# Kernel optimization log

Measured on AMD Instinct MI355X. Metric: run time of the kernel, lower is better.

## Reference

```python
import jax, jax.numpy as jnp
import numpy as np
from jax import lax

B, C, W, H = 32, 64, 32, 32
HEADS, RED = 4, 16
D = C // HEADS


def setup_inputs() -> dict:
    key = jax.random.key(0)
    ks = jax.random.split(key, 16)
    s = 0.05
    return {
        "x": jax.random.normal(ks[0], (B, C, W, H), jnp.float32),
        "Wq": jax.random.normal(ks[1], (C, C), jnp.float32) * s,
        "bq": jnp.zeros((C,), jnp.float32),
        "Wk": jax.random.normal(ks[2], (C, C), jnp.float32) * s,
        "bk": jnp.zeros((C,), jnp.float32),
        "Wv": jax.random.normal(ks[3], (C, C), jnp.float32) * s,
        "bv": jnp.zeros((C,), jnp.float32),
        "rel_h": jax.random.normal(ks[4], (1, HEADS, D, 1, H), jnp.float32),
        "rel_w": jax.random.normal(ks[5], (1, HEADS, D, W, 1), jnp.float32),
        "ln_g": jnp.ones((C, W, H), jnp.float32),
        "ln_b": jnp.zeros((C, W, H), jnp.float32),
        "ca_w1": jax.random.normal(ks[6], (C // RED, C), jnp.float32) * s,
        "ca_b1": jnp.zeros((C // RED,), jnp.float32),
        "ca_w2": jax.random.normal(ks[7], (C, C // RED), jnp.float32) * s,
        "ca_b2": jnp.zeros((C,), jnp.float32),
        "sa_w": jax.random.normal(ks[8], (1, 2, 7, 7), jnp.float32) * s,
        "sa_b": jnp.zeros((1,), jnp.float32),
    }


def reference(x, Wq, bq, Wk, bk, Wv, bv, rel_h, rel_w, ln_g, ln_b,
              ca_w1, ca_b1, ca_w2, ca_b2, sa_w, sa_b):
    b, c, w, h = x.shape
    n = w * h
    d = c // HEADS

    def conv1x1(t, wt, bt):
        return jnp.einsum('bchw,oc->bohw', t, wt) + bt[None, :, None, None]

    # ---- MHSA branch ----
    q = conv1x1(x, Wq, bq).reshape(b, HEADS, d, n)
    k = conv1x1(x, Wk, bk).reshape(b, HEADS, d, n)
    v = conv1x1(x, Wv, bv).reshape(b, HEADS, d, n)
    cc = jnp.einsum('bhdi,bhdj->bhij', q, k)                  # content-content
    pos = (rel_h + rel_w).reshape(1, HEADS, d, n)              # [1,H,d,N]
    cp = jnp.einsum('zhdi,bhdj->bhij', pos, q)                 # content-position
    att = jax.nn.softmax(cc + cp, axis=-1)                     # [b,H,N,N]
    out = jnp.einsum('bhdj,bhij->bhdi', v, att).reshape(b, c, w, h)
    # LayerNorm over (C,W,H)
    mu = jnp.mean(out, axis=(1, 2, 3), keepdims=True)
    var = jnp.var(out, axis=(1, 2, 3), keepdims=True)
    ln = (out - mu) * lax.rsqrt(var + 1e-5) * ln_g[None] + ln_b[None]
    mhsa = ln + x

    # ---- CBAM branch ----
    avg = jnp.mean(x, axis=(2, 3))                             # [b,c]
    mx = jnp.max(x, axis=(2, 3))

    def mlp(f):
        hid = jax.nn.relu(jnp.einsum('bc,oc->bo', f, ca_w1) + ca_b1)
        return jnp.einsum('bc,oc->bo', hid, ca_w2) + ca_b2

    ch_att = jax.nn.sigmoid(mlp(avg) + mlp(mx))[:, :, None, None]
    xc = ch_att * x
    feat = jnp.stack([jnp.mean(xc, axis=1), jnp.max(xc, axis=1)], axis=1)  # [b,2,w,h]
    sp = lax.conv_general_dilated(feat, sa_w, (1, 1), 'SAME',
                                  dimension_numbers=('NCHW', 'OIHW', 'NCHW'))
    sp = sp + sa_b[None, :, None, None]
    cbam = jax.nn.sigmoid(sp) * xc

    return mhsa + cbam + x
```

## Files before the change

### kernel.cpp

```cpp
#include <hip/hip_runtime.h>

#define BB 32
#define CC 64
#define WW 32
#define HHT 32
#define NH 4
#define DHD 16
#define NN 1024
#define LOG2E 1.4426950408889634f

typedef __attribute__((ext_vector_type(8))) short bf16x8;
typedef __attribute__((ext_vector_type(4))) float f32x4;

__device__ __forceinline__ float wave_sum(float v) {
#pragma unroll
  for (int off = 32; off > 0; off >>= 1) v += __shfl_down(v, off, 64);
  return v;
}
__device__ __forceinline__ float wave_max(float v) {
#pragma unroll
  for (int off = 32; off > 0; off >>= 1) v = fmaxf(v, __shfl_down(v, off, 64));
  return v;
}
__device__ __forceinline__ unsigned bf16pair(float lo, float hi) {
  unsigned a = __float_as_uint(lo), b = __float_as_uint(hi);
  a += 0x7FFFu + ((a >> 16) & 1u);
  b += 0x7FFFu + ((b >> 16) & 1u);
  return (a >> 16) | (b & 0xFFFF0000u);
}
__device__ __forceinline__ short bf16s(float f) {
  unsigned a = __float_as_uint(f);
  a += 0x7FFFu + ((a >> 16) & 1u);
  return (short)(a >> 16);
}

__global__ __launch_bounds__(256) void qkv_kernel(
    const float* __restrict__ x,
    const float* __restrict__ Wq, const float* __restrict__ bq,
    const float* __restrict__ Wk, const float* __restrict__ bk,
    const float* __restrict__ Wv, const float* __restrict__ bv,
    short* __restrict__ KQ, short* __restrict__ Vb, float* __restrict__ lnzero)
{
  __shared__ __align__(16) short Ws[192 * 72];
  const int tid = threadIdx.x;
  const int b = blockIdx.y, nt = blockIdx.x;

  if (tid < 192) {
    const int m = tid >> 4, dd = tid & 15;
    const int mat = m >> 2, h = m & 3;
    const float* src = (mat == 0 ? Wk : (mat == 1 ? Wq : Wv)) + (h * 16 + dd) * CC;
    const float scale = (mat == 0) ? LOG2E : 1.f;
    short* dst = Ws + tid * 72;
#pragma unroll
    for (int c8 = 0; c8 < 8; ++c8) {
      const float4 f0 = *reinterpret_cast<const float4*>(src + c8 * 8);
      const float4 f1 = *reinterpret_cast<const float4*>(src + c8 * 8 + 4);
      uint4 u;
      u.x = bf16pair(f0.x*scale, f0.y*scale); u.y = bf16pair(f0.z*scale, f0.w*scale);
      u.z = bf16pair(f1.x*scale, f1.y*scale); u.w = bf16pair(f1.z*scale, f1.w*scale);
      *reinterpret_cast<uint4*>(dst + c8 * 8) = u;
    }
  }
  if (blockIdx.x == 0 && blockIdx.y == 0 && tid < 64) lnzero[tid] = 0.f;
  __syncthreads();

  const int wid = tid >> 6, lane = tid & 63, Q = lane >> 4, il = lane & 15;
  const int n = nt * 64 + wid * 16 + il;
  const float* xb = x + (size_t)b * CC * NN;

  union { bf16x8 s; unsigned u[4]; } bfr[2];
#pragma unroll
  for (int half = 0; half < 2; ++half) {
#pragma unroll
    for (int p = 0; p < 4; ++p) {
      const int c0 = 32 * half + 8 * Q + 2 * p;
      const float f0 = xb[(size_t)c0 * NN + n];
      const float f1 = xb[(size_t)(c0 + 1) * NN + n];
      bfr[half].u[p] = bf16pair(f0, f1);
    }
  }

  const f32x4 zero4 = {0.f, 0.f, 0.f, 0.f};
  f32x4 acc[12];
#pragma unroll
  for (int m = 0; m < 12; ++m) {
    const short* wr = Ws + (m * 16 + il) * 72;
    const bf16x8 a0 = *reinterpret_cast<const bf16x8*>(wr + 8 * Q);
    const bf16x8 a1 = *reinterpret_cast<const bf16x8*>(wr + 32 + 8 * Q);
    acc[m] = __builtin_amdgcn_mfma_f32_16x16x32_bf16(a0, bfr[0].s, zero4, 0, 0, 0);
    acc[m] = __builtin_amdgcn_mfma_f32_16x16x32_bf16(a1, bfr[1].s, acc[m], 0, 0, 0);
  }

#pragma unroll
  for (int m = 0; m < 12; ++m) {
    const int mat = m >> 2, h = m & 3;
    const float bsc = (mat == 0) ? LOG2E : 1.f;
    const float4 bias = *reinterpret_cast<const float4*>(
        (mat == 0 ? bk : (mat == 1 ? bq : bv)) + h * 16 + 4 * Q);
    const float v0 = acc[m][0] + bias.x*bsc, v1 = acc[m][1] + bias.y*bsc;
    const float v2 = acc[m][2] + bias.z*bsc, v3 = acc[m][3] + bias.w*bsc;
    if (mat < 2) {
      uint2 pk;
      pk.x = bf16pair(v0, v1); pk.y = bf16pair(v2, v3);
      *reinterpret_cast<uint2*>(KQ + ((size_t)(b * NH + h) * NN + n) * 32 +
                                (mat == 0 ? 0 : 16) + 4 * Q) = pk;
    } else {
      short* vb = Vb + ((size_t)(b * NH + h) * 16 + 4 * Q) * NN + n;
      vb[0]            = bf16s(v0);
      vb[(size_t)NN]   = bf16s(v1);
      vb[2*(size_t)NN] = bf16s(v2);
      vb[3*(size_t)NN] = bf16s(v3);
    }
  }
}

__global__ __launch_bounds__(256, 4) void flash_kernel(
    const short* __restrict__ KQ, const short* __restrict__ Vb,
    const float* __restrict__ rel_h, const float* __restrict__ rel_w,
    float* __restrict__ attnout, float* __restrict__ lnsum, float* __restrict__ lnsum2)
{
  const int tid = threadIdx.x;
  const int wid = tid >> 6, lane = tid & 63;
  const int Q = lane >> 4, il = lane & 15;
  const int bh = blockIdx.x;
  const int h = bh & 3, b = bh >> 2;
  const int ibase = blockIdx.y * 128 + wid * 32;

  bf16x8 bfrag[2];
#pragma unroll
  for (int g2 = 0; g2 < 2; ++g2) {
    const int i = ibase + g2*16 + il;
    if (Q < 2) {
      bfrag[g2] = *reinterpret_cast<const bf16x8*>(KQ + ((size_t)bh*NN + i)*32 + 16 + 8*Q);
    } else {
      const int wrow = i >> 5, hcol = i & 31;
      union { bf16x8 s; unsigned u[4]; } t;
#pragma unroll
      for (int p = 0; p < 4; ++p) {
        const int d0 = 8*(Q-2) + 2*p;
        const float f0 = LOG2E*(rel_h[(h*DHD + d0)*HHT + hcol] + rel_w[(h*DHD + d0)*WW + wrow]);
        const float f1 = LOG2E*(rel_h[(h*DHD + d0+1)*HHT + hcol] + rel_w[(h*DHD + d0+1)*WW + wrow]);
        t.u[p] = bf16pair(f0, f1);
      }
      bfrag[g2] = t.s;
    }
  }

  const short* KQb = KQ + (size_t)bh*NN*32;
  const short* Vbb = Vb + ((size_t)bh*16 + il)*NN;
  const f32x4 zero4 = {0.f, 0.f, 0.f, 0.f};
  f32x4 acc[2]  = {zero4, zero4};
  f32x4 lacc[2] = {zero4, zero4};
  union { bf16x8 s; unsigned u[4]; } ones;
  ones.u[0] = ones.u[1] = ones.u[2] = ones.u[3] = 0x3F803F80u;

  bf16x8 agc[4]; uint2 vloc[2], vhic[2];
#pragma unroll
  for (int g = 0; g < 4; ++g)
    agc[g] = *reinterpret_cast<const bf16x8*>(KQb + (size_t)(16*g + il)*32 + 8*Q);
#pragma unroll
  for (int hh = 0; hh < 2; ++hh) {
    const short* vp = Vbb + 32*hh + 4*Q;
    vloc[hh] = *reinterpret_cast<const uint2*>(vp);
    vhic[hh] = *reinterpret_cast<const uint2*>(vp + 16);
  }

  for (int jt = 0; jt < NN; jt += 64) {
    const int jn = (jt + 64) & (NN - 1);
    bf16x8 agn[4]; uint2 vlon[2], vhin[2];
#pragma unroll
    for (int g = 0; g < 4; ++g)
      agn[g] = *reinterpret_cast<const bf16x8*>(KQb + (size_t)(jn + 16*g + il)*32 + 8*Q);
#pragma unroll
    for (int hh = 0; hh < 2; ++hh) {
      const short* vp = Vbb + jn + 32*hh + 4*Q;
      vlon[hh] = *reinterpret_cast<const uint2*>(vp);
      vhin[hh] = *reinterpret_cast<const uint2*>(vp + 16);
    }

    union { bf16x8 s; unsigned u[4]; } bv0, bv1;
    bv0.u[0] = vloc[0].x; bv0.u[1] = vloc[0].y; bv0.u[2] = vhic[0].x; bv0.u[3] = vhic[0].y;
    bv1.u[0] = vloc[1].x; bv1.u[1] = vloc[1].y; bv1.u[2] = vhic[1].x; bv1.u[3] = vhic[1].y;

#pragma unroll
    for (int g2 = 0; g2 < 2; ++g2) {
      unsigned pk[4][2];
#pragma unroll
      for (int g = 0; g < 4; ++g) {
        const f32x4 s = __builtin_amdgcn_mfma_f32_16x16x32_bf16(agc[g], bfrag[g2], zero4, 0, 0, 0);
        const float p0 = __builtin_amdgcn_exp2f(s[0]);
        const float p1 = __builtin_amdgcn_exp2f(s[1]);
        const float p2 = __builtin_amdgcn_exp2f(s[2]);
        const float p3 = __builtin_amdgcn_exp2f(s[3]);
        pk[g][0] = bf16pair(p0, p1);
        pk[g][1] = bf16pair(p2, p3);
      }
#pragma unroll
      for (int hh = 0; hh < 2; ++hh) {
        union { bf16x8 s; unsigned u[4]; } ap;
        ap.u[0] = pk[2*hh][0];   ap.u[1] = pk[2*hh][1];
        ap.u[2] = pk[2*hh+1][0]; ap.u[3] = pk[2*hh+1][1];
        acc[g2]  = __builtin_amdgcn_mfma_f32_16x16x32_bf16(ap.s, hh ? bv1.s : bv0.s, acc[g2], 0, 0, 0);
        lacc[g2] = __builtin_amdgcn_mfma_f32_16x16x32_bf16(ap.s, ones.s, lacc[g2], 0, 0, 0);
      }
    }
#pragma unroll
    for (int g = 0; g < 4; ++g) agc[g] = agn[g];
#pragma unroll
    for (int hh = 0; hh < 2; ++hh) { vloc[hh] = vlon[hh]; vhic[hh] = vhin[hh]; }
  }

  float s1 = 0.f, s2 = 0.f;
#pragma unroll
  for (int g2 = 0; g2 < 2; ++g2) {
#pragma unroll
    for (int r = 0; r < 4; ++r) {
      const float v = acc[g2][r] / lacc[g2][r];
      const int ig = ibase + g2*16 + 4*Q + r;
      attnout[((size_t)b*CC + h*DHD + il)*NN + ig] = v;
      s1 += v; s2 += v*v;
    }
  }
  s1 = wave_sum(s1); s2 = wave_sum(s2);
  __shared__ float r1[4], r2[4];
  if (lane == 0) { r1[wid] = s1; r2[wid] = s2; }
  __syncthreads();
  if (tid == 0) {
    atomicAdd(&lnsum[b],  r1[0]+r1[1]+r1[2]+r1[3]);
    atomicAdd(&lnsum2[b], r2[0]+r2[1]+r2[2]+r2[3]);
  }
}

__global__ __launch_bounds__(256) void cbamstats_kernel(
    const float* __restrict__ x, float* __restrict__ avg, float* __restrict__ mx)
{
  const int bc = blockIdx.x, tid = threadIdx.x;
  const float* p = x + (size_t)bc*NN;
  float s = 0.f, m = -3.0e38f;
  for (int u = tid; u < NN; u += 256) { const float v = p[u]; s += v; m = fmaxf(m, v); }
  s = wave_sum(s); m = wave_max(m);
  __shared__ float rs[4], rm[4];
  const int wid = tid >> 6, lane = tid & 63;
  if (lane == 0) { rs[wid] = s; rm[wid] = m; }
  __syncthreads();
  if (tid == 0) {
    avg[bc] = (rs[0]+rs[1]+rs[2]+rs[3]) * (1.f/NN);
    mx[bc]  = fmaxf(fmaxf(rm[0], rm[1]), fmaxf(rm[2], rm[3]));
  }
}

__global__ __launch_bounds__(256) void mlpfeat_kernel(
    const float* __restrict__ x, const float* __restrict__ avg, const float* __restrict__ mxv,
    const float* __restrict__ w1, const float* __restrict__ b1,
    const float* __restrict__ w2, const float* __restrict__ b2,
    float* __restrict__ chv, float* __restrict__ feat)
{
  const int b = blockIdx.y, qq = blockIdx.x, tid = threadIdx.x;
  __shared__ float sa[CC], sm[CC], sch[CC];
  __shared__ float ps[4][64], pm[4][64];
  if (tid < CC) { sa[tid] = avg[b*CC + tid]; sm[tid] = mxv[b*CC + tid]; }
  __syncthreads();
  if (tid < CC) {
    float s = 2.f * b2[tid];
#pragma unroll
    for (int o = 0; o < 4; ++o) {
      float ha = b1[o], hm = b1[o];
#pragma unroll
      for (int k = 0; k < CC; ++k) { ha += w1[o*CC + k]*sa[k]; hm += w1[o*CC + k]*sm[k]; }
      s += w2[tid*4 + o] * (fmaxf(ha, 0.f) + fmaxf(hm, 0.f));
    }
    const float c = 1.f/(1.f + __expf(-s));
    sch[tid] = c;
    if (qq == 0) chv[b*CC + tid] = c;
  }
  __syncthreads();
  const int nl = tid & 63, cg = tid >> 6;
  const int n = qq*64 + nl;
  float s = 0.f, m = -3.0e38f;
#pragma unroll
  for (int c = cg*16; c < cg*16 + 16; ++c) {
    const float v = sch[c] * x[((size_t)b*CC + c)*NN + n];
    s += v; m = fmaxf(m, v);
  }
  ps[cg][nl] = s; pm[cg][nl] = m;
  __syncthreads();
  if (cg == 0) {
    const float S = ps[0][nl]+ps[1][nl]+ps[2][nl]+ps[3][nl];
    const float M = fmaxf(fmaxf(pm[0][nl], pm[1][nl]), fmaxf(pm[2][nl], pm[3][nl]));
    feat[(size_t)b*2*NN + n]      = S * (1.f/CC);
    feat[(size_t)b*2*NN + NN + n] = M;
  }
}

__global__ __launch_bounds__(256) void final_kernel(
    const float* __restrict__ x, const float* __restrict__ attn,
    const float* __restrict__ ln_g, const float* __restrict__ ln_b,
    const float* __restrict__ feat, const float* __restrict__ ch,
    const float* __restrict__ lnsum, const float* __restrict__ lnsum2,
    const float* __restrict__ sa_w, const float* __restrict__ sa_b,
    float* __restrict__ out)
{
  const int b = blockIdx.y;
  const int c0 = blockIdx.z * 16;
  const int n = blockIdx.x*256 + threadIdx.x;
  const int w = n >> 5, hh = n & 31;
  __shared__ float sch[CC];
  __shared__ float swt[98];
  if (threadIdx.x < CC) sch[threadIdx.x] = ch[b*CC + threadIdx.x];
  if (threadIdx.x < 98) swt[threadIdx.x] = sa_w[threadIdx.x];
  __syncthreads();

  float s = sa_b[0];
#pragma unroll
  for (int ci = 0; ci < 2; ++ci)
#pragma unroll
    for (int kh = 0; kh < 7; ++kh) {
      const int wy = w + kh - 3;
      if (wy < 0 || wy >= WW) continue;
#pragma unroll
      for (int kw = 0; kw < 7; ++kw) {
        const int hx = hh + kw - 3;
        if (hx < 0 || hx >= HHT) continue;
        s += feat[((size_t)(b*2) + ci)*NN + wy*HHT + hx] * swt[ci*49 + kh*7 + kw];
      }
    }
  const float sg = 1.f/(1.f + __expf(-s));
  const float inv = 1.f/(CC*NN);
  const float m = lnsum[b]*inv;
  const float var = lnsum2[b]*inv - m*m;
  const float r = rsqrtf(var + 1e-5f);
#pragma unroll
  for (int c = c0; c < c0 + 16; ++c) {
    const size_t idx = ((size_t)b*CC + c)*NN + n;
    const float xa = x[idx];
    const float ln = (attn[idx] - m) * r * ln_g[c*NN + n] + ln_b[c*NN + n];
    out[idx] = ln + 2.f*xa + sg * sch[c] * xa;
  }
}

extern "C" void kernel_launch(void* const* d_in, const int* in_sizes, int n_in,
                              void* d_out, int out_size, void* d_ws, size_t ws_size,
                              hipStream_t stream)
{
  const float* x     = (const float*)d_in[0];
  const float* Wq    = (const float*)d_in[1];
  const float* bq    = (const float*)d_in[2];
  const float* Wk    = (const float*)d_in[3];
  const float* bk    = (const float*)d_in[4];
  const float* Wv    = (const float*)d_in[5];
  const float* bv    = (const float*)d_in[6];
  const float* rel_h = (const float*)d_in[7];
  const float* rel_w = (const float*)d_in[8];
  const float* ln_g  = (const float*)d_in[9];
  const float* ln_b  = (const float*)d_in[10];
  const float* cw1   = (const float*)d_in[11];
  const float* cb1   = (const float*)d_in[12];
  const float* cw2   = (const float*)d_in[13];
  const float* cb2   = (const float*)d_in[14];
  const float* saw   = (const float*)d_in[15];
  const float* sab   = (const float*)d_in[16];
  float* out = (float*)d_out;

  short* KQ = (short*)d_ws;
  short* Vb = KQ + (size_t)128*1024*32;
  float* fs = (float*)(Vb + (size_t)128*16*1024);
  float* lnsum  = fs;
  float* lnsum2 = fs + 32;
  float* avg    = fs + 64;
  float* mxv    = avg + 2048;
  float* chv    = mxv + 2048;
  float* feat   = chv + 2048;
  float* attn   = out;

  qkv_kernel<<<dim3(16, BB), 256, 0, stream>>>(x, Wq, bq, Wk, bk, Wv, bv, KQ, Vb, lnsum);
  flash_kernel<<<dim3(BB*NH, 8), 256, 0, stream>>>(KQ, Vb, rel_h, rel_w, attn, lnsum, lnsum2);
  cbamstats_kernel<<<BB*CC, 256, 0, stream>>>(x, avg, mxv);
  mlpfeat_kernel<<<dim3(16, BB), 256, 0, stream>>>(x, avg, mxv, cw1, cb1, cw2, cb2, chv, feat);
  final_kernel<<<dim3(4, BB, 4), 256, 0, stream>>>(x, attn, ln_g, ln_b, feat, chv, lnsum, lnsum2, saw, sab, out);
}
```

Before: 185.4 us.

## Split key range across wave pairs with 64-query tiles and LDS combine

Each wave now handles 64 query rows (four fragments) over half of the key range instead of 32 rows over all keys. Partial numerators and denominators are merged through shared memory before normalization and the LayerNorm statistics. This doubles reuse of each loaded K/V tile per wave, halving global load traffic per score. The cost is more registers per wave, an extra LDS round trip and barrier, and the loss of the explicit software prefetch of the next tile.

```diff
diff --git a/kernel.cpp b/kernel.cpp
--- a/kernel.cpp
+++ b/kernel.cpp
@@ -124,11 +124,14 @@
   const int Q = lane >> 4, il = lane & 15;
   const int bh = blockIdx.x;
   const int h = bh & 3, b = bh >> 2;
-  const int ibase = blockIdx.y * 128 + wid * 32;
-
-  bf16x8 bfrag[2];
-#pragma unroll
-  for (int g2 = 0; g2 < 2; ++g2) {
+  const int pr = wid & 1;
+  const int jh = wid >> 1;
+  const int ibase = blockIdx.y * 128 + pr * 64;
+  const int j0base = jh * 512;
+
+  bf16x8 bfrag[4];
+#pragma unroll
+  for (int g2 = 0; g2 < 4; ++g2) {
     const int i = ibase + g2*16 + il;
     if (Q < 2) {
       bfrag[g2] = *reinterpret_cast<const bf16x8*>(KQ + ((size_t)bh*NN + i)*32 + 16 + 8*Q);
@@ -149,45 +152,35 @@
   const short* KQb = KQ + (size_t)bh*NN*32;
   const short* Vbb = Vb + ((size_t)bh*16 + il)*NN;
   const f32x4 zero4 = {0.f, 0.f, 0.f, 0.f};
-  f32x4 acc[2]  = {zero4, zero4};
-  f32x4 lacc[2] = {zero4, zero4};
+  f32x4 acc[4]  = {zero4, zero4, zero4, zero4};
+  f32x4 lacc[4] = {zero4, zero4, zero4, zero4};
   union { bf16x8 s; unsigned u[4]; } ones;
   ones.u[0] = ones.u[1] = ones.u[2] = ones.u[3] = 0x3F803F80u;
 
-  bf16x8 agc[4]; uint2 vloc[2], vhic[2];
-#pragma unroll
-  for (int g = 0; g < 4; ++g)
-    agc[g] = *reinterpret_cast<const bf16x8*>(KQb + (size_t)(16*g + il)*32 + 8*Q);
-#pragma unroll
-  for (int hh = 0; hh < 2; ++hh) {
-    const short* vp = Vbb + 32*hh + 4*Q;
-    vloc[hh] = *reinterpret_cast<const uint2*>(vp);
-    vhic[hh] = *reinterpret_cast<const uint2*>(vp + 16);
-  }
-
-  for (int jt = 0; jt < NN; jt += 64) {
-    const int jn = (jt + 64) & (NN - 1);
-    bf16x8 agn[4]; uint2 vlon[2], vhin[2];
+#pragma unroll 2
+  for (int t = 0; t < 8; ++t) {
+    const int j0 = j0base + t*64;
+    bf16x8 ag[4];
 #pragma unroll
     for (int g = 0; g < 4; ++g)
-      agn[g] = *reinterpret_cast<const bf16x8*>(KQb + (size_t)(jn + 16*g + il)*32 + 8*Q);
-#pragma unroll
-    for (int hh = 0; hh < 2; ++hh) {
-      const short* vp = Vbb + jn + 32*hh + 4*Q;
-      vlon[hh] = *reinterpret_cast<const uint2*>(vp);
-      vhin[hh] = *reinterpret_cast<const uint2*>(vp + 16);
-    }
-
+      ag[g] = *reinterpret_cast<const bf16x8*>(KQb + (size_t)(j0 + 16*g + il)*32 + 8*Q);
     union { bf16x8 s; unsigned u[4]; } bv0, bv1;
-    bv0.u[0] = vloc[0].x; bv0.u[1] = vloc[0].y; bv0.u[2] = vhic[0].x; bv0.u[3] = vhic[0].y;
-    bv1.u[0] = vloc[1].x; bv1.u[1] = vloc[1].y; bv1.u[2] = vhic[1].x; bv1.u[3] = vhic[1].y;
-
-#pragma unroll
-    for (int g2 = 0; g2 < 2; ++g2) {
+    {
+      const short* vp0 = Vbb + j0 + 4*Q;
+      const uint2 l0 = *reinterpret_cast<const uint2*>(vp0);
+      const uint2 h0 = *reinterpret_cast<const uint2*>(vp0 + 16);
+      const uint2 l1 = *reinterpret_cast<const uint2*>(vp0 + 32);
+      const uint2 h1 = *reinterpret_cast<const uint2*>(vp0 + 48);
+      bv0.u[0] = l0.x; bv0.u[1] = l0.y; bv0.u[2] = h0.x; bv0.u[3] = h0.y;
+      bv1.u[0] = l1.x; bv1.u[1] = l1.y; bv1.u[2] = h1.x; bv1.u[3] = h1.y;
+    }
+
+#pragma unroll
+    for (int g2 = 0; g2 < 4; ++g2) {
       unsigned pk[4][2];
 #pragma unroll
       for (int g = 0; g < 4; ++g) {
-        const f32x4 s = __builtin_amdgcn_mfma_f32_16x16x32_bf16(agc[g], bfrag[g2], zero4, 0, 0, 0);
+        const f32x4 s = __builtin_amdgcn_mfma_f32_16x16x32_bf16(ag[g], bfrag[g2], zero4, 0, 0, 0);
         const float p0 = __builtin_amdgcn_exp2f(s[0]);
         const float p1 = __builtin_amdgcn_exp2f(s[1]);
         const float p2 = __builtin_amdgcn_exp2f(s[2]);
@@ -204,30 +197,40 @@
         lacc[g2] = __builtin_amdgcn_mfma_f32_16x16x32_bf16(ap.s, ones.s, lacc[g2], 0, 0, 0);
       }
     }
-#pragma unroll
-    for (int g = 0; g < 4; ++g) agc[g] = agn[g];
-#pragma unroll
-    for (int hh = 0; hh < 2; ++hh) { vloc[hh] = vlon[hh]; vhic[hh] = vhin[hh]; }
-  }
-
-  float s1 = 0.f, s2 = 0.f;
-#pragma unroll
-  for (int g2 = 0; g2 < 2; ++g2) {
-#pragma unroll
-    for (int r = 0; r < 4; ++r) {
-      const float v = acc[g2][r] / lacc[g2][r];
-      const int ig = ibase + g2*16 + 4*Q + r;
-      attnout[((size_t)b*CC + h*DHD + il)*NN + ig] = v;
-      s1 += v; s2 += v*v;
-    }
-  }
-  s1 = wave_sum(s1); s2 = wave_sum(s2);
-  __shared__ float r1[4], r2[4];
-  if (lane == 0) { r1[wid] = s1; r2[wid] = s2; }
+  }
+
+  __shared__ float cmb[2][32][64];
+  __shared__ float r1[2], r2[2];
+  if (jh == 1) {
+#pragma unroll
+    for (int g2 = 0; g2 < 4; ++g2)
+#pragma unroll
+      for (int r = 0; r < 4; ++r) {
+        cmb[pr][g2*4 + r][lane]      = acc[g2][r];
+        cmb[pr][16 + g2*4 + r][lane] = lacc[g2][r];
+      }
+  }
+  __syncthreads();
+  if (jh == 0) {
+    float s1 = 0.f, s2 = 0.f;
+#pragma unroll
+    for (int g2 = 0; g2 < 4; ++g2)
+#pragma unroll
+      for (int r = 0; r < 4; ++r) {
+        const float num = acc[g2][r]  + cmb[pr][g2*4 + r][lane];
+        const float den = lacc[g2][r] + cmb[pr][16 + g2*4 + r][lane];
+        const float v = num / den;
+        const int ig = ibase + g2*16 + 4*Q + r;
+        attnout[((size_t)b*CC + h*DHD + il)*NN + ig] = v;
+        s1 += v; s2 += v*v;
+      }
+    s1 = wave_sum(s1); s2 = wave_sum(s2);
+    if (lane == 0) { r1[pr] = s1; r2[pr] = s2; }
+  }
   __syncthreads();
   if (tid == 0) {
-    atomicAdd(&lnsum[b],  r1[0]+r1[1]+r1[2]+r1[3]);
-    atomicAdd(&lnsum2[b], r2[0]+r2[1]+r2[2]+r2[3]);
+    atomicAdd(&lnsum[b],  r1[0] + r1[1]);
+    atomicAdd(&lnsum2[b], r2[0] + r2[1]);
   }
 }
 
```

Result: faster. 161.4 us (-13.0%).
